# Kernel optimization log

Hardware: AMD Instinct MI355X
Metric: run time of the kernel (lower is better)

Reference implementation:

```python
import jax, jax.numpy as jnp
import numpy as np

REL_CONTEXT = 0.2  # default forward arg

def setup_inputs() -> dict:
    key = jax.random.key(0)
    ks = jax.random.split(key, 8)
    B, M, D = 4096, 2, 2048
    return {
        "x": jax.random.normal(ks[0], (B, M, D), jnp.float32),
        "sub_type_ids": jax.random.randint(ks[1], (B, M), 0, M),
        "modal_weights": jnp.ones((M,), jnp.float32),
        "emb_table": jax.random.normal(ks[2], (M, D), jnp.float32),
        "Wt": jax.random.normal(ks[3], (D, D), jnp.float32) * (1.0 / np.sqrt(D)),
        "bt": jax.random.normal(ks[4], (D,), jnp.float32) * 0.01,
        "Wrc": jax.random.normal(ks[5], (1, D), jnp.float32) * (1.0 / np.sqrt(D)),
        "brc": jax.random.normal(ks[6], (1,), jnp.float32) * 0.01,
    }

def reference(x, sub_type_ids, modal_weights, emb_table, Wt, bt, Wrc, brc):
    B = x.shape[0]
    D = emb_table.shape[1]
    x = x.reshape(B, -1, D)  # [B, M, D]
    # relational gate: Linear(D->1) on a constant vector filled with 0.2 -> scalar
    rc = jnp.full((D,), REL_CONTEXT, dtype=x.dtype)
    zeta = jax.nn.sigmoid(rc @ Wrc.T + brc)  # [1]
    sub = emb_table[sub_type_ids]  # [B, M, D] embedding lookup
    # fused: per-modality Linear + ReLU (replaces the B*M python loop)
    t = jax.nn.relu(jnp.einsum('bmd,ed->bme', x + sub, Wt) + bt)  # [B, M, D]
    h = modal_weights[None, :, None] * t * zeta[0]
    # dropout is identity in eval mode; final ReLU as in the original
    return jax.nn.relu(h)
```

## Files before the change

### kernel.cpp

```cpp
#include <hip/hip_runtime.h>
#include <hip/hip_bf16.h>
#include <math.h>

#define MROWS 8192
#define KDIM  2048
#define NDIM  2048

#define BM 256
#define BN 256
#define BK 64
#define NT (KDIM / BK)

typedef short  v8s __attribute__((ext_vector_type(8)));
typedef float  v4f __attribute__((ext_vector_type(4)));

#define A_OFF   0ull
#define W_OFF   ((unsigned long long)MROWS * KDIM * 2ull)
#define MWZ_OFF (W_OFF + (unsigned long long)NDIM * KDIM * 2ull)

__device__ inline unsigned short f2bf(float f) {
    __hip_bfloat16 h = __float2bfloat16(f);
    return *reinterpret_cast<unsigned short*>(&h);
}

__global__ __launch_bounds__(256) void prep_kernel(
    const float* __restrict__ x, const int* __restrict__ ids,
    const float* __restrict__ mw, const float* __restrict__ emb,
    const float* __restrict__ Wrc, const float* __restrict__ brc,
    const float* __restrict__ Wt,
    unsigned short* __restrict__ Abf, unsigned short* __restrict__ Wbf,
    float* __restrict__ mwz)
{
    const int tid = threadIdx.x;

    if (blockIdx.x == 0) {
        __shared__ float red[256];
        float s = 0.f;
        for (int d = tid; d < KDIM; d += 256) s += Wrc[d];
        red[tid] = s;
        __syncthreads();
        for (int off = 128; off > 0; off >>= 1) {
            if (tid < off) red[tid] += red[tid + off];
            __syncthreads();
        }
        if (tid == 0) {
            float zeta = 1.0f / (1.0f + expf(-(0.2f * red[0] + brc[0])));
            mwz[0] = mw[0] * zeta;
            mwz[1] = mw[1] * zeta;
        }
    }

    const int groupsA = MROWS * KDIM / 8;
    for (int g = blockIdx.x * 256 + tid; g < groupsA; g += gridDim.x * 256) {
        const int row = g >> 8;
        const int off = (g & 255) << 3;
        const int st  = ids[row];
        const float4* xp = (const float4*)(x   + (size_t)row * KDIM + off);
        const float4* ep = (const float4*)(emb + (size_t)st  * KDIM + off);
        float4 x0 = xp[0], x1 = xp[1];
        float4 e0 = ep[0], e1 = ep[1];
        v8s o;
        o[0] = (short)f2bf(x0.x + e0.x);
        o[1] = (short)f2bf(x0.y + e0.y);
        o[2] = (short)f2bf(x0.z + e0.z);
        o[3] = (short)f2bf(x0.w + e0.w);
        o[4] = (short)f2bf(x1.x + e1.x);
        o[5] = (short)f2bf(x1.y + e1.y);
        o[6] = (short)f2bf(x1.z + e1.z);
        o[7] = (short)f2bf(x1.w + e1.w);
        *(v8s*)(Abf + (size_t)g * 8) = o;
    }

    const int groupsW = NDIM * KDIM / 8;
    for (int g = blockIdx.x * 256 + tid; g < groupsW; g += gridDim.x * 256) {
        const float4* wp = (const float4*)(Wt + (size_t)g * 8);
        float4 w0 = wp[0], w1 = wp[1];
        v8s o;
        o[0] = (short)f2bf(w0.x); o[1] = (short)f2bf(w0.y);
        o[2] = (short)f2bf(w0.z); o[3] = (short)f2bf(w0.w);
        o[4] = (short)f2bf(w1.x); o[5] = (short)f2bf(w1.y);
        o[6] = (short)f2bf(w1.z); o[7] = (short)f2bf(w1.w);
        *(v8s*)(Wbf + (size_t)g * 8) = o;
    }
}


#define SBAR()   __builtin_amdgcn_s_barrier()
#define LGKM0()  asm volatile("s_waitcnt lgkmcnt(0)" ::: "memory")
#define VMCNT(n) asm volatile("s_waitcnt vmcnt(" #n ")" ::: "memory")

template<int P>
__device__ __forceinline__ void mfma_phase(v4f (&acc)[8][4],
                                           const v8s (&b)[4][2],
                                           const v8s (&a)[2][2])
{
    __builtin_amdgcn_s_setprio(1);
    #pragma unroll
    for (int j = 0; j < 4; ++j) {
        acc[2*P  ][j] = __builtin_amdgcn_mfma_f32_16x16x32_bf16(b[j][0], a[0][0], acc[2*P  ][j], 0, 0, 0);
        acc[2*P+1][j] = __builtin_amdgcn_mfma_f32_16x16x32_bf16(b[j][0], a[1][0], acc[2*P+1][j], 0, 0, 0);
    }
    #pragma unroll
    for (int j = 0; j < 4; ++j) {
        acc[2*P  ][j] = __builtin_amdgcn_mfma_f32_16x16x32_bf16(b[j][1], a[0][1], acc[2*P  ][j], 0, 0, 0);
        acc[2*P+1][j] = __builtin_amdgcn_mfma_f32_16x16x32_bf16(b[j][1], a[1][1], acc[2*P+1][j], 0, 0, 0);
    }
    __builtin_amdgcn_s_setprio(0);
}

#define KTILE(CA, CB, OA, T)                                              \
  {                                                                       \
    v8s a[2][2], b[4][2];                                                 \
    b[0][0] = rdB(CB, 0, 0); b[0][1] = rdB(CB, 0, 1);                     \
    b[1][0] = rdB(CB, 1, 0); b[1][1] = rdB(CB, 1, 1);                     \
    b[2][0] = rdB(CB, 2, 0); b[2][1] = rdB(CB, 2, 1);                     \
    b[3][0] = rdB(CB, 3, 0); b[3][1] = rdB(CB, 3, 1);                     \
    a[0][0] = rdA(CA, 0, 0); a[0][1] = rdA(CA, 0, 1);                     \
    a[1][0] = rdA(CA, 1, 0); a[1][1] = rdA(CA, 1, 1);                     \
    stage(OA, gA, (T) + 1, 1); stage(OA, gA, (T) + 1, 3);                 \
    SBAR(); mfma_phase<0>(acc, b, a); LGKM0(); SBAR();                    \
    a[0][0] = rdA(CA, 2, 0); a[0][1] = rdA(CA, 2, 1);                     \
    a[1][0] = rdA(CA, 3, 0); a[1][1] = rdA(CA, 3, 1);                     \
    stage(CB, gB, (T) + 2, 0); stage(CB, gB, (T) + 2, 1);                 \
    SBAR(); mfma_phase<1>(acc, b, a); LGKM0(); VMCNT(10); SBAR();         \
    a[0][0] = rdA(CA, 4, 0); a[0][1] = rdA(CA, 4, 1);                     \
    a[1][0] = rdA(CA, 5, 0); a[1][1] = rdA(CA, 5, 1);                     \
    stage(CB, gB, (T) + 2, 2); stage(CB, gB, (T) + 2, 3);                 \
    SBAR(); mfma_phase<2>(acc, b, a); LGKM0(); SBAR();                    \
    a[0][0] = rdA(CA, 6, 0); a[0][1] = rdA(CA, 6, 1);                     \
    a[1][0] = rdA(CA, 7, 0); a[1][1] = rdA(CA, 7, 1);                     \
    stage(CA, gA, (T) + 2, 0); stage(CA, gA, (T) + 2, 2);                 \
    SBAR(); mfma_phase<3>(acc, b, a); LGKM0(); VMCNT(8); SBAR();          \
  }

__global__ __launch_bounds__(512, 2) void gemm_kernel(
    const unsigned short* __restrict__ Abf,
    const unsigned short* __restrict__ Wbf,
    const float* __restrict__ bt,
    const float* __restrict__ mwz,
    float* __restrict__ out)
{
    __shared__ __align__(16) unsigned short lA0[BM * BK];
    __shared__ __align__(16) unsigned short lA1[BM * BK];
    __shared__ __align__(16) unsigned short lB0[BN * BK];
    __shared__ __align__(16) unsigned short lB1[BN * BK];

    const int tid  = threadIdx.x;
    const int lane = tid & 63;
    const int wave = tid >> 6;
    const int wr   = wave & 1;
    const int wc   = wave >> 1;
    const int quad = lane >> 4;
    const int mcol = lane & 15;

    const int br = blockIdx.x;
    const int bc = blockIdx.y;

    const unsigned short* gA = Abf + (size_t)(br * BM) * KDIM;
    const unsigned short* gB = Wbf + (size_t)(bc * BN) * KDIM;

    v4f acc[8][4];
    const v4f vzero = {0.f, 0.f, 0.f, 0.f};
    #pragma unroll
    for (int i = 0; i < 8; i++)
        #pragma unroll
        for (int j = 0; j < 4; j++) acc[i][j] = vzero;

    auto stage = [&](unsigned short* dst, const unsigned short* gsrc,
                     int t, int s) {
        const int f   = (s << 9) + tid;
        const int row = f >> 3;
        const int ch  = (f & 7) ^ (row & 7);
        const unsigned short* g = gsrc + (size_t)row * KDIM + ((t & 31) << 6) + (ch << 3);
        __builtin_amdgcn_global_load_lds(
            (const __attribute__((address_space(1))) void*)g,
            (__attribute__((address_space(3))) void*)(dst + ((size_t)f << 3)),
            16, 0, 0);
    };

    auto rdA = [&](const unsigned short* l, int i, int ks) -> v8s {
        const int row = (wr << 7) + (i << 4) + mcol;
        const int c   = ((ks << 2) + quad) ^ (row & 7);
        return *(const v8s*)(l + (row << 6) + (c << 3));
    };
    auto rdB = [&](const unsigned short* l, int j, int ks) -> v8s {
        const int col = (wc << 6) + (j << 4) + mcol;
        const int c   = ((ks << 2) + quad) ^ (col & 7);
        return *(const v8s*)(l + (col << 6) + (c << 3));
    };

    stage(lB0, gB, 0, 0); stage(lB0, gB, 0, 1);
    stage(lB0, gB, 0, 2); stage(lB0, gB, 0, 3);
    stage(lA0, gA, 0, 0); stage(lA0, gA, 0, 2);
    stage(lA0, gA, 0, 1); stage(lA0, gA, 0, 3);
    stage(lB1, gB, 1, 0); stage(lB1, gB, 1, 1);
    stage(lB1, gB, 1, 2); stage(lB1, gB, 1, 3);
    stage(lA1, gA, 1, 0); stage(lA1, gA, 1, 2);
    VMCNT(8);
    SBAR();

    #pragma unroll 1
    for (int tt = 0; tt < NT; tt += 2) {
        KTILE(lA0, lB0, lA1, tt);
        KTILE(lA1, lB1, lA0, tt + 1);
    }

    const float mz = mwz[mcol & 1];
    #pragma unroll
    for (int j = 0; j < 4; ++j) {
        const int ncol = bc * BN + wc * 64 + j * 16 + quad * 4;
        const float4 b4 = *(const float4*)(bt + ncol);
        #pragma unroll
        for (int i = 0; i < 8; ++i) {
            const int row = br * BM + wr * 128 + i * 16 + mcol;
            float4 o;
            o.x = fmaxf(mz * fmaxf(acc[i][j][0] + b4.x, 0.0f), 0.0f);
            o.y = fmaxf(mz * fmaxf(acc[i][j][1] + b4.y, 0.0f), 0.0f);
            o.z = fmaxf(mz * fmaxf(acc[i][j][2] + b4.z, 0.0f), 0.0f);
            o.w = fmaxf(mz * fmaxf(acc[i][j][3] + b4.w, 0.0f), 0.0f);
            *(float4*)(out + (size_t)row * NDIM + ncol) = o;
        }
    }
}

extern "C" void kernel_launch(void* const* d_in, const int* in_sizes, int n_in,
                              void* d_out, int out_size, void* d_ws, size_t ws_size,
                              hipStream_t stream) {
    const float* x    = (const float*)d_in[0];
    const int*   ids  = (const int*)  d_in[1];
    const float* mw   = (const float*)d_in[2];
    const float* emb  = (const float*)d_in[3];
    const float* Wt   = (const float*)d_in[4];
    const float* bt   = (const float*)d_in[5];
    const float* Wrc  = (const float*)d_in[6];
    const float* brc  = (const float*)d_in[7];
    float* out = (float*)d_out;

    char* ws = (char*)d_ws;
    unsigned short* Abf = (unsigned short*)(ws + A_OFF);
    unsigned short* Wbf = (unsigned short*)(ws + W_OFF);
    float* mwz          = (float*)(ws + MWZ_OFF);

    prep_kernel<<<2048, 256, 0, stream>>>(x, ids, mw, emb, Wrc, brc, Wt,
                                          Abf, Wbf, mwz);

    dim3 grid(MROWS / BM, NDIM / BN);
    gemm_kernel<<<grid, 512, 0, stream>>>(Abf, Wbf, bt, mwz, out);
}
```

Measured before the change: 202.2 us.

## Fuse prep conversion and GEMM into one cooperative kernel with grid sync

Merges the bf16 conversion/embedding-add prep pass and the GEMM into a single cooperative launch, separated by a grid-wide barrier. The GEMM grid of 256 blocks of 512 threads now also performs the prep work in a grid-stride loop. This is meant to remove the second kernel launch and the gap between the two kernels. In exchange it uses a cooperative launch and a grid sync, which need all 256 blocks to be co-resident. The prep phase also runs with fewer blocks than before and with the GEMM kernel's register and LDS footprint, which may lower the occupancy available to it.

```diff
diff --git a/kernel.cpp b/kernel.cpp
--- a/kernel.cpp
+++ b/kernel.cpp
@@ -1,4 +1,5 @@
 #include <hip/hip_runtime.h>
+#include <hip/hip_cooperative_groups.h>
 #include <hip/hip_bf16.h>
 #include <math.h>
 
@@ -22,68 +23,6 @@
     __hip_bfloat16 h = __float2bfloat16(f);
     return *reinterpret_cast<unsigned short*>(&h);
 }
-
-__global__ __launch_bounds__(256) void prep_kernel(
-    const float* __restrict__ x, const int* __restrict__ ids,
-    const float* __restrict__ mw, const float* __restrict__ emb,
-    const float* __restrict__ Wrc, const float* __restrict__ brc,
-    const float* __restrict__ Wt,
-    unsigned short* __restrict__ Abf, unsigned short* __restrict__ Wbf,
-    float* __restrict__ mwz)
-{
-    const int tid = threadIdx.x;
-
-    if (blockIdx.x == 0) {
-        __shared__ float red[256];
-        float s = 0.f;
-        for (int d = tid; d < KDIM; d += 256) s += Wrc[d];
-        red[tid] = s;
-        __syncthreads();
-        for (int off = 128; off > 0; off >>= 1) {
-            if (tid < off) red[tid] += red[tid + off];
-            __syncthreads();
-        }
-        if (tid == 0) {
-            float zeta = 1.0f / (1.0f + expf(-(0.2f * red[0] + brc[0])));
-            mwz[0] = mw[0] * zeta;
-            mwz[1] = mw[1] * zeta;
-        }
-    }
-
-    const int groupsA = MROWS * KDIM / 8;
-    for (int g = blockIdx.x * 256 + tid; g < groupsA; g += gridDim.x * 256) {
-        const int row = g >> 8;
-        const int off = (g & 255) << 3;
-        const int st  = ids[row];
-        const float4* xp = (const float4*)(x   + (size_t)row * KDIM + off);
-        const float4* ep = (const float4*)(emb + (size_t)st  * KDIM + off);
-        float4 x0 = xp[0], x1 = xp[1];
-        float4 e0 = ep[0], e1 = ep[1];
-        v8s o;
-        o[0] = (short)f2bf(x0.x + e0.x);
-        o[1] = (short)f2bf(x0.y + e0.y);
-        o[2] = (short)f2bf(x0.z + e0.z);
-        o[3] = (short)f2bf(x0.w + e0.w);
-        o[4] = (short)f2bf(x1.x + e1.x);
-        o[5] = (short)f2bf(x1.y + e1.y);
-        o[6] = (short)f2bf(x1.z + e1.z);
-        o[7] = (short)f2bf(x1.w + e1.w);
-        *(v8s*)(Abf + (size_t)g * 8) = o;
-    }
-
-    const int groupsW = NDIM * KDIM / 8;
-    for (int g = blockIdx.x * 256 + tid; g < groupsW; g += gridDim.x * 256) {
-        const float4* wp = (const float4*)(Wt + (size_t)g * 8);
-        float4 w0 = wp[0], w1 = wp[1];
-        v8s o;
-        o[0] = (short)f2bf(w0.x); o[1] = (short)f2bf(w0.y);
-        o[2] = (short)f2bf(w0.z); o[3] = (short)f2bf(w0.w);
-        o[4] = (short)f2bf(w1.x); o[5] = (short)f2bf(w1.y);
-        o[6] = (short)f2bf(w1.z); o[7] = (short)f2bf(w1.w);
-        *(v8s*)(Wbf + (size_t)g * 8) = o;
-    }
-}
-
 
 #define SBAR()   __builtin_amdgcn_s_barrier()
 #define LGKM0()  asm volatile("s_waitcnt lgkmcnt(0)" ::: "memory")
@@ -107,6 +46,7 @@
     }
     __builtin_amdgcn_s_setprio(0);
 }
+
 
 #define KTILE(CA, CB, OA, T)                                              \
   {                                                                       \
@@ -133,19 +73,75 @@
     SBAR(); mfma_phase<3>(acc, b, a); LGKM0(); VMCNT(8); SBAR();          \
   }
 
-__global__ __launch_bounds__(512, 2) void gemm_kernel(
-    const unsigned short* __restrict__ Abf,
-    const unsigned short* __restrict__ Wbf,
-    const float* __restrict__ bt,
-    const float* __restrict__ mwz,
-    float* __restrict__ out)
+__global__ __launch_bounds__(512, 2) void fused_kernel(
+    const float* __restrict__ x, const int* __restrict__ ids,
+    const float* __restrict__ mw, const float* __restrict__ emb,
+    const float* __restrict__ Wrc, const float* __restrict__ brc,
+    const float* __restrict__ Wt, const float* __restrict__ bt,
+    unsigned short* __restrict__ Abf, unsigned short* __restrict__ Wbf,
+    float* __restrict__ mwz, float* __restrict__ out)
 {
+    const int tid   = threadIdx.x;
+    const int flatb = blockIdx.y * gridDim.x + blockIdx.x;
+
+    if (flatb == 0) {
+        __shared__ float red[512];
+        float s = 0.f;
+        for (int d = tid; d < KDIM; d += 512) s += Wrc[d];
+        red[tid] = s;
+        __syncthreads();
+        for (int off = 256; off > 0; off >>= 1) {
+            if (tid < off) red[tid] += red[tid + off];
+            __syncthreads();
+        }
+        if (tid == 0) {
+            float zeta = 1.0f / (1.0f + expf(-(0.2f * red[0] + brc[0])));
+            mwz[0] = mw[0] * zeta;
+            mwz[1] = mw[1] * zeta;
+        }
+    }
+
+    const int groupsA = MROWS * KDIM / 8;
+    for (int g = flatb * 512 + tid; g < groupsA; g += 256 * 512) {
+        const int row = g >> 8;
+        const int off = (g & 255) << 3;
+        const int st  = ids[row];
+        const float4* xp = (const float4*)(x   + (size_t)row * KDIM + off);
+        const float4* ep = (const float4*)(emb + (size_t)st  * KDIM + off);
+        float4 x0 = xp[0], x1 = xp[1];
+        float4 e0 = ep[0], e1 = ep[1];
+        v8s o;
+        o[0] = (short)f2bf(x0.x + e0.x);
+        o[1] = (short)f2bf(x0.y + e0.y);
+        o[2] = (short)f2bf(x0.z + e0.z);
+        o[3] = (short)f2bf(x0.w + e0.w);
+        o[4] = (short)f2bf(x1.x + e1.x);
+        o[5] = (short)f2bf(x1.y + e1.y);
+        o[6] = (short)f2bf(x1.z + e1.z);
+        o[7] = (short)f2bf(x1.w + e1.w);
+        *(v8s*)(Abf + (size_t)g * 8) = o;
+    }
+
+    const int groupsW = NDIM * KDIM / 8;
+    for (int g = flatb * 512 + tid; g < groupsW; g += 256 * 512) {
+        const float4* wp = (const float4*)(Wt + (size_t)g * 8);
+        float4 w0 = wp[0], w1 = wp[1];
+        v8s o;
+        o[0] = (short)f2bf(w0.x); o[1] = (short)f2bf(w0.y);
+        o[2] = (short)f2bf(w0.z); o[3] = (short)f2bf(w0.w);
+        o[4] = (short)f2bf(w1.x); o[5] = (short)f2bf(w1.y);
+        o[6] = (short)f2bf(w1.z); o[7] = (short)f2bf(w1.w);
+        *(v8s*)(Wbf + (size_t)g * 8) = o;
+    }
+
+    __threadfence();
+    cooperative_groups::this_grid().sync();
+
     __shared__ __align__(16) unsigned short lA0[BM * BK];
     __shared__ __align__(16) unsigned short lA1[BM * BK];
     __shared__ __align__(16) unsigned short lB0[BN * BK];
     __shared__ __align__(16) unsigned short lB1[BN * BK];
 
-    const int tid  = threadIdx.x;
     const int lane = tid & 63;
     const int wave = tid >> 6;
     const int wr   = wave & 1;
@@ -241,9 +237,11 @@
     unsigned short* Wbf = (unsigned short*)(ws + W_OFF);
     float* mwz          = (float*)(ws + MWZ_OFF);
 
-    prep_kernel<<<2048, 256, 0, stream>>>(x, ids, mw, emb, Wrc, brc, Wt,
-                                          Abf, Wbf, mwz);
-
-    dim3 grid(MROWS / BM, NDIM / BN);
-    gemm_kernel<<<grid, 512, 0, stream>>>(Abf, Wbf, bt, mwz, out);
-}
+    void* args[] = { (void*)&x, (void*)&ids, (void*)&mw, (void*)&emb,
+                     (void*)&Wrc, (void*)&brc, (void*)&Wt, (void*)&bt,
+                     (void*)&Abf, (void*)&Wbf, (void*)&mwz, (void*)&out };
+
+    hipLaunchCooperativeKernel((const void*)fused_kernel,
+                               dim3(MROWS / BM, NDIM / BN), dim3(512),
+                               args, 0, stream);
+}
```

After: 327.6 us. +62.0%, slower.
